# Performance work log

Measured on AMD Instinct MI355X. Metric: run time of the kernel, lower is better.

## Reference

```python
import jax, jax.numpy as jnp
import numpy as np
from jax import lax

C = 128  # channels after deconv_2

def _deconvs(x, w1, b1, w2, b2):
    # x: (N,512,4,4)
    N = x.shape[0]
    # ConvTranspose2d k=1 s=2: 4 -> 7; values land on even positions, bias elsewhere
    z1 = jnp.einsum('nchw,co->nohw', x, w1)  # (N,256,4,4)
    h1 = jnp.broadcast_to(b1[None, :, None, None], (N, 256, 7, 7))
    h1 = h1.at[:, :, ::2, ::2].set(z1 + b1[None, :, None, None])
    # ConvTranspose2d k=1 s=2 pad=1: 7 -> 11; full output 13 at even idx, crop 1 each side
    # -> input positions 1..5 land at output odd positions 1,3,5,7,9
    z2 = jnp.einsum('nchw,co->nohw', h1, w2)  # (N,128,7,7)
    feat = jnp.broadcast_to(b2[None, :, None, None], (N, C, 11, 11))
    feat = feat.at[:, :, 1::2, 1::2].set(z2[:, :, 1:6, 1:6] + b2[None, :, None, None])
    return feat  # (N,128,11,11)

def _categorize(rois):
    r = rois.astype(jnp.int32)
    y0, x0, y1, x1 = r[:, 0], r[:, 1], r[:, 2], r[:, 3]
    inb = jnp.all((r >= 0) & (r < 11), axis=1)
    h, w = y1 - y0, x1 - x0
    cat = jnp.where(inb & (h == 4) & (w == 4), 0,
          jnp.where(inb & (h == 8) & (w == 8), 1,
          jnp.where(inb & (h == 4) & (w == 8), 2,
          jnp.where(inb & (h == 6) & (w == 8), 3, 4))))
    # invalid anchors -> forced crop (1,1,10,10) i.e. 9x9 starting at (1,1)
    y0 = jnp.where(cat == 4, 1, y0)
    x0 = jnp.where(cat == 4, 1, x0)
    return y0, x0, cat

def _pool_one(f, y0, x0, cat):
    # f: (128,11,11); compute all 5 pooling candidates, select by category
    neg = jnp.finfo(f.dtype).min
    c0 = lax.dynamic_slice(f, (0, y0, x0), (C, 4, 4))                    # identity
    s88 = lax.dynamic_slice(f, (0, y0, x0), (C, 8, 8))
    c1 = s88.reshape(C, 4, 2, 4, 2).max(axis=(2, 4))                    # 2x2 s2
    s48 = lax.dynamic_slice(f, (0, y0, x0), (C, 4, 8))
    c2 = s48.reshape(C, 4, 4, 2).max(axis=3)                            # 1d pool k2
    s68 = lax.dynamic_slice(f, (0, y0, x0), (C, 6, 8))
    p68 = jnp.pad(s68, ((0, 0), (1, 1), (0, 0)), constant_values=neg)   # pad H by 1
    c3 = p68.reshape(C, 4, 2, 4, 2).max(axis=(2, 4))                    # 2x2 s2 padH1
    s99 = lax.dynamic_slice(f, (0, y0, x0), (C, 9, 9))
    c4 = lax.reduce_window(s99, neg, lax.max, (1, 3, 3), (1, 2, 2), 'VALID')  # 3x3 s2
    return jnp.stack([c0, c1, c2, c3, c4])[cat]

def reference(base_feat, rois, w1, b1, w2, b2, wl, bl):
    B = base_feat.shape[0]
    x = base_feat.reshape(-1, 512, 4, 4)
    feat = _deconvs(x, w1, b1, w2, b2)          # (N,128,11,11)
    y0, x0, cat = _categorize(rois)
    pooled = jax.vmap(_pool_one)(feat, y0, x0, cat)   # (N,128,4,4)
    h = pooled.reshape(B, -1, 2048) @ wl + bl         # (B,R,1024)
    return jnp.where(h > 0, h, 0.01 * h)              # LeakyReLU(0.01)

def setup_inputs():
    key = jax.random.key(0)
    ks = jax.random.split(key, 8)
    B, R = 32, 256
    N = B * R
    return {
        'base_feat': jax.random.normal(ks[0], (B, R, 512, 4, 4), jnp.float32),
        'rois': jax.random.randint(ks[1], (N, 4), 0, 12, jnp.int32),
        'w1': jax.random.normal(ks[2], (512, 256), jnp.float32) * 0.02,
        'b1': jax.random.normal(ks[3], (256,), jnp.float32) * 0.02,
        'w2': jax.random.normal(ks[4], (256, 128), jnp.float32) * 0.02,
        'b2': jax.random.normal(ks[5], (128,), jnp.float32) * 0.02,
        'wl': jax.random.normal(ks[6], (2048, 1024), jnp.float32) * 0.02,
        'bl': jax.random.normal(ks[7], (1024,), jnp.float32) * 0.02,
    }
```

## Files before the change

### kernel.cpp

```cpp
#include <hip/hip_runtime.h>
#include <float.h>
#include <stdint.h>

typedef __attribute__((ext_vector_type(8))) short bf16x8;
typedef __attribute__((ext_vector_type(4))) float f32x4;

__device__ __forceinline__ unsigned short f2bf(float f) {
  unsigned u = __builtin_bit_cast(unsigned, f);
  u += 0x7fffu + ((u >> 16) & 1u);
  return (unsigned short)(u >> 16);
}

__device__ __forceinline__ void gl_lds16(const void* g, void* s) {
  __builtin_amdgcn_global_load_lds(
      (const __attribute__((address_space(1))) unsigned int*)(uintptr_t)g,
      (__attribute__((address_space(3))) unsigned int*)(unsigned int)(uintptr_t)s,
      16, 0, 0);
}

__global__ void k_prep_wt(const float* __restrict__ w1, const float* __restrict__ w2,
                          unsigned short* __restrict__ Wt) {
  int tid = blockIdx.x * 256 + threadIdx.x;
  int o = tid & 127;
  int kc = tid >> 7;
  for (int kk = 0; kk < 4; ++kk) {
    int k = kc * 4 + kk;
    const float* w1r = w1 + k * 256;
    float a0 = 0.f, a1 = 0.f;
    for (int c = 0; c < 256; c += 2) {
      a0 += w1r[c] * w2[c * 128 + o];
      a1 += w1r[c + 1] * w2[(c + 1) * 128 + o];
    }
    Wt[o * 512 + k] = f2bf(a0 + a1);
  }
}

__global__ void k_prep_dval(const float* __restrict__ b1, const float* __restrict__ w2,
                            const float* __restrict__ b2, float* __restrict__ dval) {
  int o = threadIdx.x;
  float acc = 0.f;
  for (int c = 0; c < 256; ++c) acc += b1[c] * w2[c * 128 + o];
  dval[o] = acc + b2[o];
}

__device__ __forceinline__ int cellmask(int cat, int y0, int x0, int i, int j) {
  int ys[3], xs[3];
  int ny, nx;
  switch (cat) {
    case 0: ys[0] = y0 + i; ny = 1; xs[0] = x0 + j; nx = 1; break;
    case 1: ys[0] = y0 + 2 * i; ys[1] = ys[0] + 1; ny = 2;
            xs[0] = x0 + 2 * j; xs[1] = xs[0] + 1; nx = 2; break;
    case 2: ys[0] = y0 + i; ny = 1;
            xs[0] = x0 + 2 * j; xs[1] = xs[0] + 1; nx = 2; break;
    case 3: if (i == 0) { ys[0] = y0; ny = 1; }
            else if (i == 3) { ys[0] = y0 + 5; ny = 1; }
            else { ys[0] = y0 + 2 * i - 1; ys[1] = y0 + 2 * i; ny = 2; }
            xs[0] = x0 + 2 * j; xs[1] = xs[0] + 1; nx = 2; break;
    default: ys[0] = 1 + 2 * i; ys[1] = 2 + 2 * i; ys[2] = 3 + 2 * i; ny = 3;
             xs[0] = 1 + 2 * j; xs[1] = 2 + 2 * j; xs[2] = 3 + 2 * j; nx = 3; break;
  }
  int m = 0;
  for (int a = 0; a < ny; ++a)
    for (int b = 0; b < nx; ++b) {
      int y = ys[a], xx = xs[b];
      if ((y & 1) && (xx & 1)) {
        if ((y == 3 || y == 7) && (xx == 3 || xx == 7))
          m |= 1 << (2 + ((y == 7) ? 2 : 0) + ((xx == 7) ? 1 : 0));
        else
          m |= 2;
      } else {
        m |= 1;
      }
    }
  return m;
}

__global__ void k_prep_mask(const int* __restrict__ rois, unsigned char* __restrict__ masks) {
  int n = blockIdx.x * 256 + threadIdx.x;
  const int* rr = rois + n * 4;
  int y0 = rr[0], x0 = rr[1], y1 = rr[2], x1 = rr[3];
  bool inb = ((unsigned)y0 < 11u) && ((unsigned)x0 < 11u) &&
             ((unsigned)y1 < 11u) && ((unsigned)x1 < 11u);
  int h = y1 - y0, ww = x1 - x0;
  int cat;
  if (inb && h == 4 && ww == 4) cat = 0;
  else if (inb && h == 8 && ww == 8) cat = 1;
  else if (inb && h == 4 && ww == 8) cat = 2;
  else if (inb && h == 6 && ww == 8) cat = 3;
  else { cat = 4; y0 = 1; x0 = 1; }
  union { unsigned char b[16]; uint4 q; } u;
  for (int cell = 0; cell < 16; ++cell)
    u.b[cell] = (unsigned char)cellmask(cat, y0, x0, cell >> 2, cell & 3);
  *(uint4*)(masks + n * 16) = u.q;
}

__global__ __launch_bounds__(256) void k_prep_wlt(const float* __restrict__ wl,
                                                  unsigned short* __restrict__ wlT) {
  __shared__ float tile[64][65];
  int b = blockIdx.x;
  int c = b & 15;
  int o0 = ((b >> 4) & 1) * 64;
  int m0 = (b >> 5) * 64;
  int t = threadIdx.x;
  int tl = t & 63, th = t >> 6;
  for (int s = 0; s < 16; ++s) {
    int ol = s * 4 + th;
    tile[ol][tl] = wl[((o0 + ol) * 16 + c) * 1024 + m0 + tl];
  }
  __syncthreads();
  for (int s = 0; s < 16; ++s) {
    int ml = s * 4 + th;
    wlT[(size_t)(m0 + ml) * 2048 + c * 128 + o0 + tl] = f2bf(tile[tl][ml]);
  }
}

__global__ __launch_bounds__(256) void k_dgemm_pool(
    const float* __restrict__ x,
    const unsigned short* __restrict__ Wt,
    const float* __restrict__ dval, const float* __restrict__ b2,
    const unsigned char* __restrict__ masks,
    unsigned short* __restrict__ pooled)
{
  __shared__ __align__(16) unsigned short As[64 * 64];
  __shared__ __align__(16) unsigned short Bs[128 * 64];
  const int t = threadIdx.x;
  const int bm = blockIdx.x;
  const int n0 = bm * 16;
  const int w = t >> 6, lane = t & 63;
  const int wm = (w >> 1) * 32, wn = (w & 1) * 64;
  const int lrow = lane & 15, lk = (lane >> 4) * 8;

  f32x4 acc[2][4];
  const f32x4 z = {0.f, 0.f, 0.f, 0.f};
  for (int i = 0; i < 2; ++i) for (int j = 0; j < 4; ++j) acc[i][j] = z;

  const int brow = t >> 1, bhalf = (t & 1) * 32;
  for (int k0 = 0; k0 < 512; k0 += 64) {
    {
      const unsigned short* gp = Wt + brow * 512 + k0 + bhalf;
      uint4 q0 = *(const uint4*)(gp + 0);
      uint4 q1 = *(const uint4*)(gp + 8);
      uint4 q2 = *(const uint4*)(gp + 16);
      uint4 q3 = *(const uint4*)(gp + 24);
      unsigned short* sp = Bs + brow * 64 + bhalf;
      *(uint4*)(sp + 0)  = q0;
      *(uint4*)(sp + 8)  = q1;
      *(uint4*)(sp + 16) = q2;
      *(uint4*)(sp + 24) = q3;
    }
#pragma unroll
    for (int s = 0; s < 4; ++s) {
      int li = s * 256 + t;
      int nl = li >> 6;
      int k = li & 63;
      const float* gp = x + (size_t)(n0 + nl) * 8192 + (size_t)(k0 + k) * 16;
      float4 qa = *(const float4*)(gp + 4);
      float4 qb = *(const float4*)(gp + 8);
      unsigned short* sp = As + nl * 256 + k;
      sp[0]   = f2bf(qa.y);
      sp[64]  = f2bf(qa.z);
      sp[128] = f2bf(qb.y);
      sp[192] = f2bf(qb.z);
    }
    __syncthreads();
#pragma unroll
    for (int kk = 0; kk < 64; kk += 32) {
      bf16x8 a[2], b[4];
      for (int i = 0; i < 2; ++i)
        a[i] = *(const bf16x8*)&As[(wm + i * 16 + lrow) * 64 + kk + lk];
      for (int j = 0; j < 4; ++j)
        b[j] = *(const bf16x8*)&Bs[(wn + j * 16 + lrow) * 64 + kk + lk];
      for (int i = 0; i < 2; ++i)
        for (int j = 0; j < 4; ++j)
          acc[i][j] = __builtin_amdgcn_mfma_f32_16x16x32_bf16(a[i], b[j], acc[i][j], 0, 0, 0);
    }
    __syncthreads();
  }

  const int lr = lane >> 4, lc = lane & 15;
  for (int i = 0; i < 2; ++i) {
    int n = n0 + (wm >> 2) + i * 4 + lr;
    uint4 mq = *(const uint4*)(masks + n * 16);
    const unsigned char* mb = (const unsigned char*)&mq;
    for (int j = 0; j < 4; ++j) {
      int o = wn + j * 16 + lc;
      float dv = dval[o], bv = b2[o];
      float d0 = acc[i][j][0] + dv, d1 = acc[i][j][1] + dv;
      float d2 = acc[i][j][2] + dv, d3 = acc[i][j][3] + dv;
      unsigned short* op = pooled + (size_t)n * 2048 + o;
#pragma unroll
      for (int cell = 0; cell < 16; ++cell) {
        int m = mb[cell];
        float v = (m & 1) ? bv : -FLT_MAX;
        if (m & 2)  v = fmaxf(v, dv);
        if (m & 4)  v = fmaxf(v, d0);
        if (m & 8)  v = fmaxf(v, d1);
        if (m & 16) v = fmaxf(v, d2);
        if (m & 32) v = fmaxf(v, d3);
        op[cell * 128] = f2bf(v);
      }
    }
  }
}

__global__ __launch_bounds__(256) void k_gemm(
    const unsigned short* __restrict__ A,
    const unsigned short* __restrict__ B,
    const float* __restrict__ bias,
    float* __restrict__ C)
{
  __shared__ __align__(16) unsigned short As[128 * 64];
  __shared__ __align__(16) unsigned short Bs[128 * 64];
  const int t = threadIdx.x;
  const int r0 = blockIdx.x * 128, c0 = blockIdx.y * 128;
  const int w = t >> 6, lane = t & 63;
  const int wm = (w >> 1) * 64, wn = (w & 1) * 64;
  const int lrow = lane & 15, lk = (lane >> 4) * 8;

  f32x4 acc[4][4];
  const f32x4 z = {0.f, 0.f, 0.f, 0.f};
  for (int i = 0; i < 4; ++i) for (int j = 0; j < 4; ++j) acc[i][j] = z;

  const int srow = lane >> 3;
  const int scol = (lane & 7) * 8;
  const unsigned short* Ag = A + (size_t)(r0 + w * 32 + srow) * 2048 + scol;
  const unsigned short* Bg = B + (size_t)(c0 + w * 32 + srow) * 2048 + scol;
  unsigned short* Asb = As + (w * 32) * 64;
  unsigned short* Bsb = Bs + (w * 32) * 64;

  for (int k0 = 0; k0 < 2048; k0 += 64) {
#pragma unroll
    for (int c = 0; c < 4; ++c) {
      gl_lds16(Ag + (size_t)c * 8 * 2048 + k0, Asb + c * 8 * 64);
      gl_lds16(Bg + (size_t)c * 8 * 2048 + k0, Bsb + c * 8 * 64);
    }
    __syncthreads();
#pragma unroll
    for (int kk = 0; kk < 64; kk += 32) {
      bf16x8 a[4], b[4];
      for (int i = 0; i < 4; ++i)
        a[i] = *(const bf16x8*)&As[(wm + i * 16 + lrow) * 64 + kk + lk];
      for (int j = 0; j < 4; ++j)
        b[j] = *(const bf16x8*)&Bs[(wn + j * 16 + lrow) * 64 + kk + lk];
      for (int i = 0; i < 4; ++i)
        for (int j = 0; j < 4; ++j)
          acc[i][j] = __builtin_amdgcn_mfma_f32_16x16x32_bf16(a[i], b[j], acc[i][j], 0, 0, 0);
    }
    __syncthreads();
  }

  const int rbase = r0 + wm + (lane >> 4) * 4;
  for (int j = 0; j < 4; ++j) {
    int col = c0 + wn + j * 16 + (lane & 15);
    float bv = bias[col];
    for (int i = 0; i < 4; ++i) {
      for (int r = 0; r < 4; ++r) {
        int row = rbase + i * 16 + r;
        float v = acc[i][j][r] + bv;
        C[(size_t)row * 1024 + col] = v > 0.f ? v : 0.01f * v;
      }
    }
  }
}

extern "C" void kernel_launch(void* const* d_in, const int* in_sizes, int n_in,
                              void* d_out, int out_size, void* d_ws, size_t ws_size,
                              hipStream_t stream) {
  const float* base_feat = (const float*)d_in[0];
  const int*   rois      = (const int*)d_in[1];
  const float* w1        = (const float*)d_in[2];
  const float* b1        = (const float*)d_in[3];
  const float* w2        = (const float*)d_in[4];
  const float* b2        = (const float*)d_in[5];
  const float* wl        = (const float*)d_in[6];
  const float* bl        = (const float*)d_in[7];
  float* out = (float*)d_out;

  char* ws = (char*)d_ws;
  unsigned short* Wt     = (unsigned short*)(ws + 0);
  float*          dval   = (float*)(ws + 131072);
  unsigned char*  masks  = (unsigned char*)(ws + 131584);
  unsigned short* pooled = (unsigned short*)(ws + 262656);
  unsigned short* wlT    = (unsigned short*)(ws + 33817088);

  k_prep_wt   <<<dim3(64),   dim3(256), 0, stream>>>(w1, w2, Wt);
  k_prep_dval <<<dim3(1),    dim3(128), 0, stream>>>(b1, w2, b2, dval);
  k_prep_mask <<<dim3(32),   dim3(256), 0, stream>>>(rois, masks);
  k_prep_wlt  <<<dim3(512),  dim3(256), 0, stream>>>(wl, wlT);
  k_dgemm_pool<<<dim3(512),  dim3(256), 0, stream>>>(base_feat, Wt, dval, b2, masks, pooled);
  k_gemm      <<<dim3(64, 8), dim3(256), 0, stream>>>(pooled, wlT, bl, out);
}
```

Before: 542.3 us.

## Merge prep kernels into one launch and XOR-swizzle LDS tiles in final GEMM

The four small preprocessing kernels (weight fold, bias fold, ROI masks, wl transpose) become one kernel that dispatches on block index, cutting three launches and the gaps between them. Separately, the final GEMM stores its A and B tiles in LDS with an XOR swizzle on the 16-byte chunk index, and reads them back with the matching swizzled offsets, to avoid LDS bank conflicts on the MFMA operand loads. The merged kernel keeps the 64x65 shared tile for every block even where it is unused, and the swizzle adds a little index arithmetic.

```diff
diff --git a/kernel.cpp b/kernel.cpp
--- a/kernel.cpp
+++ b/kernel.cpp
@@ -16,31 +16,6 @@
       (const __attribute__((address_space(1))) unsigned int*)(uintptr_t)g,
       (__attribute__((address_space(3))) unsigned int*)(unsigned int)(uintptr_t)s,
       16, 0, 0);
-}
-
-__global__ void k_prep_wt(const float* __restrict__ w1, const float* __restrict__ w2,
-                          unsigned short* __restrict__ Wt) {
-  int tid = blockIdx.x * 256 + threadIdx.x;
-  int o = tid & 127;
-  int kc = tid >> 7;
-  for (int kk = 0; kk < 4; ++kk) {
-    int k = kc * 4 + kk;
-    const float* w1r = w1 + k * 256;
-    float a0 = 0.f, a1 = 0.f;
-    for (int c = 0; c < 256; c += 2) {
-      a0 += w1r[c] * w2[c * 128 + o];
-      a1 += w1r[c + 1] * w2[(c + 1) * 128 + o];
-    }
-    Wt[o * 512 + k] = f2bf(a0 + a1);
-  }
-}
-
-__global__ void k_prep_dval(const float* __restrict__ b1, const float* __restrict__ w2,
-                            const float* __restrict__ b2, float* __restrict__ dval) {
-  int o = threadIdx.x;
-  float acc = 0.f;
-  for (int c = 0; c < 256; ++c) acc += b1[c] * w2[c * 128 + o];
-  dval[o] = acc + b2[o];
 }
 
 __device__ __forceinline__ int cellmask(int cat, int y0, int x0, int i, int j) {
@@ -75,42 +50,67 @@
   return m;
 }
 
-__global__ void k_prep_mask(const int* __restrict__ rois, unsigned char* __restrict__ masks) {
-  int n = blockIdx.x * 256 + threadIdx.x;
-  const int* rr = rois + n * 4;
-  int y0 = rr[0], x0 = rr[1], y1 = rr[2], x1 = rr[3];
-  bool inb = ((unsigned)y0 < 11u) && ((unsigned)x0 < 11u) &&
-             ((unsigned)y1 < 11u) && ((unsigned)x1 < 11u);
-  int h = y1 - y0, ww = x1 - x0;
-  int cat;
-  if (inb && h == 4 && ww == 4) cat = 0;
-  else if (inb && h == 8 && ww == 8) cat = 1;
-  else if (inb && h == 4 && ww == 8) cat = 2;
-  else if (inb && h == 6 && ww == 8) cat = 3;
-  else { cat = 4; y0 = 1; x0 = 1; }
-  union { unsigned char b[16]; uint4 q; } u;
-  for (int cell = 0; cell < 16; ++cell)
-    u.b[cell] = (unsigned char)cellmask(cat, y0, x0, cell >> 2, cell & 3);
-  *(uint4*)(masks + n * 16) = u.q;
-}
-
-__global__ __launch_bounds__(256) void k_prep_wlt(const float* __restrict__ wl,
-                                                  unsigned short* __restrict__ wlT) {
+__global__ __launch_bounds__(256) void k_prep(
+    const float* __restrict__ w1, const float* __restrict__ b1,
+    const float* __restrict__ w2, const float* __restrict__ b2,
+    const float* __restrict__ wl, const int* __restrict__ rois,
+    unsigned short* __restrict__ Wt, float* __restrict__ dval,
+    unsigned char* __restrict__ masks, unsigned short* __restrict__ wlT)
+{
   __shared__ float tile[64][65];
-  int b = blockIdx.x;
-  int c = b & 15;
-  int o0 = ((b >> 4) & 1) * 64;
-  int m0 = (b >> 5) * 64;
-  int t = threadIdx.x;
-  int tl = t & 63, th = t >> 6;
-  for (int s = 0; s < 16; ++s) {
-    int ol = s * 4 + th;
-    tile[ol][tl] = wl[((o0 + ol) * 16 + c) * 1024 + m0 + tl];
-  }
-  __syncthreads();
-  for (int s = 0; s < 16; ++s) {
-    int ml = s * 4 + th;
-    wlT[(size_t)(m0 + ml) * 2048 + c * 128 + o0 + tl] = f2bf(tile[tl][ml]);
+  const int blk = blockIdx.x;
+  const int t = threadIdx.x;
+  if (blk < 512) {
+    int c = blk & 15;
+    int o0 = ((blk >> 4) & 1) * 64;
+    int m0 = (blk >> 5) * 64;
+    int tl = t & 63, th = t >> 6;
+    for (int s = 0; s < 16; ++s) {
+      int ol = s * 4 + th;
+      tile[ol][tl] = wl[((o0 + ol) * 16 + c) * 1024 + m0 + tl];
+    }
+    __syncthreads();
+    for (int s = 0; s < 16; ++s) {
+      int ml = s * 4 + th;
+      wlT[(size_t)(m0 + ml) * 2048 + c * 128 + o0 + tl] = f2bf(tile[tl][ml]);
+    }
+  } else if (blk < 576) {
+    int tid = (blk - 512) * 256 + t;
+    int o = tid & 127;
+    int kc = tid >> 7;
+    for (int kk = 0; kk < 4; ++kk) {
+      int k = kc * 4 + kk;
+      const float* w1r = w1 + k * 256;
+      float a0 = 0.f, a1 = 0.f;
+      for (int c = 0; c < 256; c += 2) {
+        a0 += w1r[c] * w2[c * 128 + o];
+        a1 += w1r[c + 1] * w2[(c + 1) * 128 + o];
+      }
+      Wt[o * 512 + k] = f2bf(a0 + a1);
+    }
+  } else if (blk < 608) {
+    int n = (blk - 576) * 256 + t;
+    const int* rr = rois + n * 4;
+    int y0 = rr[0], x0 = rr[1], y1 = rr[2], x1 = rr[3];
+    bool inb = ((unsigned)y0 < 11u) && ((unsigned)x0 < 11u) &&
+               ((unsigned)y1 < 11u) && ((unsigned)x1 < 11u);
+    int h = y1 - y0, ww = x1 - x0;
+    int cat;
+    if (inb && h == 4 && ww == 4) cat = 0;
+    else if (inb && h == 8 && ww == 8) cat = 1;
+    else if (inb && h == 4 && ww == 8) cat = 2;
+    else if (inb && h == 6 && ww == 8) cat = 3;
+    else { cat = 4; y0 = 1; x0 = 1; }
+    union { unsigned char b[16]; uint4 q; } u;
+    for (int cell = 0; cell < 16; ++cell)
+      u.b[cell] = (unsigned char)cellmask(cat, y0, x0, cell >> 2, cell & 3);
+    *(uint4*)(masks + n * 16) = u.q;
+  } else {
+    if (t < 128) {
+      float acc = 0.f;
+      for (int c = 0; c < 256; ++c) acc += b1[c] * w2[c * 128 + t];
+      dval[t] = acc + b2[t];
+    }
   }
 }
 
@@ -222,12 +222,21 @@
   for (int i = 0; i < 4; ++i) for (int j = 0; j < 4; ++j) acc[i][j] = z;
 
   const int srow = lane >> 3;
-  const int scol = (lane & 7) * 8;
+  const int scol = ((lane & 7) ^ srow) * 8;
   const unsigned short* Ag = A + (size_t)(r0 + w * 32 + srow) * 2048 + scol;
   const unsigned short* Bg = B + (size_t)(c0 + w * 32 + srow) * 2048 + scol;
   unsigned short* Asb = As + (w * 32) * 64;
   unsigned short* Bsb = Bs + (w * 32) * 64;
 
+  int sw[2][4];
+#pragma unroll
+  for (int kh = 0; kh < 2; ++kh)
+#pragma unroll
+    for (int q = 0; q < 4; ++q)
+      sw[kh][q] = (((kh * 4 + q) ^ (lrow & 7)) * 8);
+
+  const int myq = lk >> 3;
+
   for (int k0 = 0; k0 < 2048; k0 += 64) {
 #pragma unroll
     for (int c = 0; c < 4; ++c) {
@@ -237,11 +246,12 @@
     __syncthreads();
 #pragma unroll
     for (int kk = 0; kk < 64; kk += 32) {
+      const int off = sw[kk >> 5][myq];
       bf16x8 a[4], b[4];
       for (int i = 0; i < 4; ++i)
-        a[i] = *(const bf16x8*)&As[(wm + i * 16 + lrow) * 64 + kk + lk];
+        a[i] = *(const bf16x8*)&As[(wm + i * 16 + lrow) * 64 + off];
       for (int j = 0; j < 4; ++j)
-        b[j] = *(const bf16x8*)&Bs[(wn + j * 16 + lrow) * 64 + kk + lk];
+        b[j] = *(const bf16x8*)&Bs[(wn + j * 16 + lrow) * 64 + off];
       for (int i = 0; i < 4; ++i)
         for (int j = 0; j < 4; ++j)
           acc[i][j] = __builtin_amdgcn_mfma_f32_16x16x32_bf16(a[i], b[j], acc[i][j], 0, 0, 0);
@@ -283,10 +293,8 @@
   unsigned short* pooled = (unsigned short*)(ws + 262656);
   unsigned short* wlT    = (unsigned short*)(ws + 33817088);
 
-  k_prep_wt   <<<dim3(64),   dim3(256), 0, stream>>>(w1, w2, Wt);
-  k_prep_dval <<<dim3(1),    dim3(128), 0, stream>>>(b1, w2, b2, dval);
-  k_prep_mask <<<dim3(32),   dim3(256), 0, stream>>>(rois, masks);
-  k_prep_wlt  <<<dim3(512),  dim3(256), 0, stream>>>(wl, wlT);
+  k_prep      <<<dim3(609),  dim3(256), 0, stream>>>(w1, b1, w2, b2, wl, rois,
+                                                     Wt, dval, masks, wlT);
   k_dgemm_pool<<<dim3(512),  dim3(256), 0, stream>>>(base_feat, Wt, dval, b2, masks, pooled);
   k_gemm      <<<dim3(64, 8), dim3(256), 0, stream>>>(pooled, wlT, bl, out);
 }
```

Result: faster. 500.8 us (-7.7%).
